# Performance work log

Hardware: AMD Instinct MI355X
Metric: run time of the kernel (lower is better)

## Reference

```python
import jax, jax.numpy as jnp
import numpy as np

B, T, F, H = 2048, 512, 60, 7  # batch, seq_len, input_size, hidden_size


def setup_inputs() -> dict:
    key = jax.random.key(0)
    ks = jax.random.split(key, 9)
    bound = 1.0 / np.sqrt(H)  # PyTorch LSTM init: U(-1/sqrt(H), 1/sqrt(H))
    u = lambda k, s: jax.random.uniform(k, s, jnp.float32, -bound, bound)
    return {
        "x": jax.random.normal(ks[0], (B, T, F), jnp.float32),
        "Wih0": u(ks[1], (4 * H, F)),
        "Whh0": u(ks[2], (4 * H, H)),
        "bih0": u(ks[3], (4 * H,)),
        "bhh0": u(ks[4], (4 * H,)),
        "Wih1": u(ks[5], (4 * H, H)),
        "Whh1": u(ks[6], (4 * H, H)),
        "bih1": u(ks[7], (4 * H,)),
        "bhh1": u(ks[8], (4 * H,)),
    }


def _cell(xt, h, c, Wih, Whh, b):
    # PyTorch gate order: input, forget, cell(g), output
    gates = xt @ Wih.T + h @ Whh.T + b  # [B, 4H]
    i, f, g, o = jnp.split(gates, 4, axis=-1)
    c_new = jax.nn.sigmoid(f) * c + jax.nn.sigmoid(i) * jnp.tanh(g)
    h_new = jax.nn.sigmoid(o) * jnp.tanh(c_new)
    return h_new, c_new


def reference(x, Wih0, Whh0, bih0, bhh0, Wih1, Whh1, bih1, bhh1):
    b0 = bih0 + bhh0
    b1 = bih1 + bhh1
    batch = x.shape[0]
    hid = Whh0.shape[1]
    z = jnp.zeros((batch, hid), x.dtype)

    def step(carry, xt):
        h0, c0, h1, c1 = carry
        h0, c0 = _cell(xt, h0, c0, Wih0, Whh0, b0)
        h1, c1 = _cell(h0, h1, c1, Wih1, Whh1, b1)
        return (h0, c0, h1, c1), None

    xs = jnp.swapaxes(x, 0, 1)  # [T, B, F] for scan over time
    (h0, c0, h1, c1), _ = jax.lax.scan(step, (z, z, z, z), xs)
    # out[:, -1] of batch_first LSTM == final hidden state of top layer
    return h1
```

## Files before the change

kernel.cpp:

```cpp
#include <hip/hip_runtime.h>


#define B_ 2048
#define T_ 512
#define F_ 60
#define H_ 7
#define G4 28
#define BT_ (B_ * T_)
#define L2E 1.4426950408889634f
#define PD 8

#if __has_builtin(__builtin_amdgcn_exp2f)
#define EXP2(x) __builtin_amdgcn_exp2f(x)
#else
#define EXP2(x) exp2f(x)
#endif

__device__ __forceinline__ float rcpf_(float v) { return __builtin_amdgcn_rcpf(v); }

__device__ __forceinline__ float bcast(float v, int srclane) {
    return __uint_as_float(__builtin_amdgcn_readlane(__float_as_uint(v), srclane));
}

__device__ __forceinline__ float dot7(const float* w, const float* h, float seed) {
    float m01 = fmaf(w[1], h[1], w[0] * h[0]);
    float m23 = fmaf(w[3], h[3], w[2] * h[2]);
    float m45 = fmaf(w[5], h[5], w[4] * h[4]);
    float m6  = fmaf(w[6], h[6], seed);
    return (m01 + m23) + (m45 + m6);
}

__global__ __launch_bounds__(256)
void proj_kernel(const float* __restrict__ x, const float* __restrict__ Wih0,
                 const float* __restrict__ bih0, const float* __restrict__ bhh0,
                 float* __restrict__ A)
{
    __shared__ float wsm[G4 * F_];
    __shared__ float bsm[G4];

    for (int i = threadIdx.x; i < G4 * F_; i += 256) wsm[i] = Wih0[i];
    if (threadIdx.x < G4) bsm[threadIdx.x] = bih0[threadIdx.x] + bhh0[threadIdx.x];
    __syncthreads();

    const int bt = blockIdx.x * 256 + threadIdx.x;

    float xr[F_];
    const float4* __restrict__ xp = (const float4*)(x + (size_t)bt * F_);
    #pragma unroll
    for (int j = 0; j < 15; ++j) {
        float4 q = xp[j];
        xr[4 * j + 0] = q.x; xr[4 * j + 1] = q.y;
        xr[4 * j + 2] = q.z; xr[4 * j + 3] = q.w;
    }

    float4* __restrict__ Ap = (float4*)(A + (size_t)bt * G4);
    #pragma unroll
    for (int rg = 0; rg < 7; ++rg) {
        float s[4];
        #pragma unroll
        for (int q = 0; q < 4; ++q) {
            const int r = rg * 4 + q;
            const float* w = &wsm[r * F_];
            float a0 = bsm[r], a1 = 0.f, a2 = 0.f, a3 = 0.f;
            #pragma unroll
            for (int k = 0; k < F_; k += 4) {
                a0 = fmaf(w[k + 0], xr[k + 0], a0);
                a1 = fmaf(w[k + 1], xr[k + 1], a1);
                a2 = fmaf(w[k + 2], xr[k + 2], a2);
                a3 = fmaf(w[k + 3], xr[k + 3], a3);
            }
            s[q] = (a0 + a1) + (a2 + a3);
        }
        Ap[rg] = make_float4(s[0], s[1], s[2], s[3]);
    }
}

__global__ __launch_bounds__(256)
void rec_kernel(const float* __restrict__ A,
                const float* __restrict__ Whh0,
                const float* __restrict__ Wih1, const float* __restrict__ Whh1,
                const float* __restrict__ bih1, const float* __restrict__ bhh1,
                float* __restrict__ out)
{
    const int tid   = threadIdx.x;
    const int lane  = tid & 63;
    const bool isL1 = lane >= 32;
    const int g     = lane & 31;
    const int r     = (g < G4) ? g : (G4 - 1);
    const int b     = blockIdx.x * 4 + (tid >> 6);

    float wA[H_], wB[H_];
    #pragma unroll
    for (int v = 0; v < H_; ++v) {
        wA[v] = isL1 ? Wih1[r * H_ + v] : Whh0[r * H_ + v];
        wB[v] = isL1 ? Whh1[r * H_ + v] : 0.f;
    }
    const float bias1 = bih1[r] + bhh1[r];

    const bool isT = (r >= 2 * H_ && r < 3 * H_);
    const float KK = isT ? (-2.f * L2E) : (-L2E);
    const float Aa = isT ? 2.f : 1.f;
    const float Ca = isT ? -1.f : 0.f;

    float h0v[H_] = {0, 0, 0, 0, 0, 0, 0};
    float h1v[H_] = {0, 0, 0, 0, 0, 0, 0};
    float c = 0.f, hnew = 0.f;

    const float* __restrict__ pa = A + (size_t)b * T_ * G4 + r;

    float buf[PD];
    #pragma unroll
    for (int i = 0; i < PD; ++i) buf[i] = pa[i * G4];

    for (int tt = 0; tt < T_; tt += PD) {
        #pragma unroll
        for (int s = 0; s < PD; ++s) {
            const int t = tt + s;
            const int tn = (t + PD < T_) ? (t + PD) : (T_ - 1);
            float nb = pa[(size_t)tn * G4];

            float seed = isL1 ? bias1 : buf[s];
            float a = dot7(wA, h0v, seed);
            a = dot7(wB, h1v, a);
            float act = fmaf(Aa, rcpf_(1.f + EXP2(KK * a)), Ca);

            float fg = __shfl(act, lane + 7, 64);
            float gg = __shfl(act, lane + 14, 64);
            float og = __shfl(act, lane + 21, 64);

            float cnew = fmaf(fg, c, act * gg);
            if (t == 0) cnew = isL1 ? 0.f : cnew;
            c = cnew;
            float th = fmaf(2.f, rcpf_(1.f + EXP2(-2.f * L2E * c)), -1.f);
            hnew = og * th;

            #pragma unroll
            for (int v = 0; v < H_; ++v) h0v[v] = bcast(hnew, v);
            #pragma unroll
            for (int v = 0; v < H_; ++v) h1v[v] = bcast(hnew, 32 + v);

            buf[s] = nb;
        }
    }

    {
        float a = dot7(wA, h0v, isL1 ? bias1 : 0.f);
        a = dot7(wB, h1v, a);
        float act = fmaf(Aa, rcpf_(1.f + EXP2(KK * a)), Ca);
        float fg = __shfl(act, lane + 7, 64);
        float gg = __shfl(act, lane + 14, 64);
        float og = __shfl(act, lane + 21, 64);
        c = fmaf(fg, c, act * gg);
        float th = fmaf(2.f, rcpf_(1.f + EXP2(-2.f * L2E * c)), -1.f);
        hnew = og * th;
    }

    if (isL1 && g < H_) out[(size_t)b * H_ + g] = hnew;
}

#define CH 16
#define NCH (T_ / CH)
#define F4 15
#define ROW4 (CH * F4)
#define BPB 4
#define TOT4 (BPB * ROW4)

__device__ __forceinline__ float proj32(const float* pw, const float4* rp, float seed) {
    float s0 = seed, s1 = 0.f, s2 = 0.f, s3 = 0.f;
    #pragma unroll
    for (int j = 0; j < 8; ++j) {
        float4 q = rp[j];
        s0 = fmaf(pw[4 * j + 0], q.x, s0);
        s1 = fmaf(pw[4 * j + 1], q.y, s1);
        s2 = fmaf(pw[4 * j + 2], q.z, s2);
        s3 = fmaf(pw[4 * j + 3], q.w, s3);
    }
    return (s0 + s1) + (s2 + s3);
}

__global__ __launch_bounds__(256, 2)
void lstm2_fallback(const float* __restrict__ x,
                    const float* __restrict__ Wih0, const float* __restrict__ Whh0,
                    const float* __restrict__ bih0, const float* __restrict__ bhh0,
                    const float* __restrict__ Wih1, const float* __restrict__ Whh1,
                    const float* __restrict__ bih1, const float* __restrict__ bhh1,
                    float* __restrict__ out)
{
    __shared__ float4 lds4[2][BPB][ROW4];

    const int tid   = threadIdx.x;
    const int lane  = tid & 63;
    const bool isL1 = lane >= 32;
    const int g     = lane & 31;
    const int r     = (g < G4) ? g : (G4 - 1);
    const int grp   = tid >> 6;
    const int b     = blockIdx.x * BPB + grp;

    float pw[32];
    {
        const int offs = isL1 ? 28 : 0;
        #pragma unroll
        for (int k = 0; k < 32; ++k) pw[k] = Wih0[r * F_ + offs + k];
        if (isL1) { pw[0] = pw[1] = pw[2] = pw[3] = 0.f; }
    }
    float wA[H_], wB[H_];
    #pragma unroll
    for (int v = 0; v < H_; ++v) {
        wA[v] = isL1 ? Wih1[r * H_ + v] : Whh0[r * H_ + v];
        wB[v] = isL1 ? Whh1[r * H_ + v] : 0.f;
    }
    const float bias0 = bih0[r] + bhh0[r];
    const float bias1 = bih1[r] + bhh1[r];

    const bool isT = (r >= 2 * H_ && r < 3 * H_);
    const float KK = isT ? (-2.f * L2E) : (-L2E);
    const float Aa = isT ? 2.f : 1.f;
    const float Ca = isT ? -1.f : 0.f;

    float h0v[H_] = {0, 0, 0, 0, 0, 0, 0};
    float h1v[H_] = {0, 0, 0, 0, 0, 0, 0};
    float c = 0.f, hnew = 0.f;

    const float4* __restrict__ xb =
        (const float4*)(x + (size_t)(blockIdx.x * BPB) * T_ * F_);
    const int XB4 = T_ * F4;
    const int lofs = isL1 ? 7 : 0;
    const float pseed = isL1 ? 0.f : bias0;

    #pragma unroll
    for (int i = 0; i < 4; ++i) {
        int idx = tid + 256 * i;
        if (idx < TOT4) {
            int bl = idx / ROW4;
            int j  = idx - bl * ROW4;
            lds4[0][bl][j] = xb[bl * XB4 + j];
        }
    }
    __syncthreads();

    float a_in;
    {
        float ow = proj32(pw, &lds4[0][grp][0] + lofs, pseed);
        a_in = ow + __shfl(ow, lane ^ 32, 64);
    }

    for (int ch = 0; ch < NCH; ++ch) {
        const int cn = (ch < NCH - 1) ? ch + 1 : ch;
        float4 st[4];
        #pragma unroll
        for (int i = 0; i < 4; ++i) {
            int idx = tid + 256 * i;
            if (idx < TOT4) {
                int bl = idx / ROW4;
                int j  = idx - bl * ROW4;
                st[i] = xb[bl * XB4 + cn * ROW4 + j];
            }
        }

        const int buf = ch & 1;
        const float4* __restrict__ rowb = &lds4[buf][grp][0] + lofs;

        #pragma unroll
        for (int s = 0; s < CH; ++s) {
            float seed = isL1 ? bias1 : a_in;
            float a = dot7(wA, h0v, seed);
            a = dot7(wB, h1v, a);
            float act = fmaf(Aa, rcpf_(1.f + EXP2(KK * a)), Ca);

            float fg = __shfl(act, lane + 7, 64);
            float gg = __shfl(act, lane + 14, 64);
            float og = __shfl(act, lane + 21, 64);

            float cnew = fmaf(fg, c, act * gg);
            if (ch == 0 && s == 0) cnew = isL1 ? 0.f : cnew;
            c = cnew;
            float th = fmaf(2.f, rcpf_(1.f + EXP2(-2.f * L2E * c)), -1.f);
            hnew = og * th;

            #pragma unroll
            for (int v = 0; v < H_; ++v) h0v[v] = bcast(hnew, v);
            if (ch > 0 || s > 0) {
                #pragma unroll
                for (int v = 0; v < H_; ++v) h1v[v] = bcast(hnew, 32 + v);
            }

            if (s < CH - 1) {
                float ow = proj32(pw, rowb + (s + 1) * F4, pseed);
                a_in = ow + __shfl(ow, lane ^ 32, 64);
            }
        }

        #pragma unroll
        for (int i = 0; i < 4; ++i) {
            int idx = tid + 256 * i;
            if (idx < TOT4) {
                int bl = idx / ROW4;
                int j  = idx - bl * ROW4;
                lds4[buf ^ 1][bl][j] = st[i];
            }
        }
        __syncthreads();

        if (ch < NCH - 1) {
            float ow = proj32(pw, &lds4[buf ^ 1][grp][0] + lofs, pseed);
            a_in = ow + __shfl(ow, lane ^ 32, 64);
        }
    }

    {
        float a = dot7(wA, h0v, isL1 ? bias1 : 0.f);
        a = dot7(wB, h1v, a);
        float act = fmaf(Aa, rcpf_(1.f + EXP2(KK * a)), Ca);
        float fg = __shfl(act, lane + 7, 64);
        float gg = __shfl(act, lane + 14, 64);
        float og = __shfl(act, lane + 21, 64);
        c = fmaf(fg, c, act * gg);
        float th = fmaf(2.f, rcpf_(1.f + EXP2(-2.f * L2E * c)), -1.f);
        hnew = og * th;
    }

    if (isL1 && g < H_) out[(size_t)b * H_ + g] = hnew;
}

extern "C" void kernel_launch(void* const* d_in, const int* in_sizes, int n_in,
                              void* d_out, int out_size, void* d_ws, size_t ws_size,
                              hipStream_t stream) {
    const float* x    = (const float*)d_in[0];
    const float* Wih0 = (const float*)d_in[1];
    const float* Whh0 = (const float*)d_in[2];
    const float* bih0 = (const float*)d_in[3];
    const float* bhh0 = (const float*)d_in[4];
    const float* Wih1 = (const float*)d_in[5];
    const float* Whh1 = (const float*)d_in[6];
    const float* bih1 = (const float*)d_in[7];
    const float* bhh1 = (const float*)d_in[8];
    float* out = (float*)d_out;

    const size_t need = (size_t)BT_ * G4 * sizeof(float);
    if (ws_size >= need) {
        float* A = (float*)d_ws;
        proj_kernel<<<dim3(BT_ / 256), dim3(256), 0, stream>>>(x, Wih0, bih0, bhh0, A);
        rec_kernel<<<dim3(B_ / 4), dim3(256), 0, stream>>>(A, Whh0, Wih1, Whh1,
                                                           bih1, bhh1, out);
    } else {
        lstm2_fallback<<<dim3(B_ / BPB), dim3(256), 0, stream>>>(
            x, Wih0, Whh0, bih0, bhh0, Wih1, Whh1, bih1, bhh1, out);
    }
}
```

Baseline: 541.0 us.

## Fuse input projection into recurrent kernel with producer/consumer warp specialization

Replaces the separate projection kernel and its global workspace with one fused kernel. Four producer waves compute the input projection for 64-step chunks into double-buffered LDS while four recurrence waves consume the previous chunk. This removes the global write and read-back of the projected gates (about 117 MB). The cost is a block-wide barrier every chunk, and the serial recurrence now depends on the producer keeping pace. Each producer lane computes a 28x60 dot product per timestep, and grid occupancy is limited to 512 blocks.

Measured after the change: 923.5 us. 1.71x slower.

```diff
diff --git a/kernel.cpp b/kernel.cpp
--- a/kernel.cpp
+++ b/kernel.cpp
@@ -6,9 +6,10 @@
 #define F_ 60
 #define H_ 7
 #define G4 28
-#define BT_ (B_ * T_)
 #define L2E 1.4426950408889634f
-#define PD 8
+#define PD 4
+#define CHK 64
+#define NCHK (T_ / CHK)
 
 #if __has_builtin(__builtin_amdgcn_exp2f)
 #define EXP2(x) __builtin_amdgcn_exp2f(x)
@@ -30,120 +31,135 @@
     return (m01 + m23) + (m45 + m6);
 }
 
-__global__ __launch_bounds__(256)
-void proj_kernel(const float* __restrict__ x, const float* __restrict__ Wih0,
-                 const float* __restrict__ bih0, const float* __restrict__ bhh0,
-                 float* __restrict__ A)
+__device__ __forceinline__ void produce(const float* __restrict__ x,
+                                        const float* __restrict__ wsm,
+                                        const float* __restrict__ bsm,
+                                        float (*__restrict__ dst)[G4],
+                                        int bb, int ck, int lane)
 {
-    __shared__ float wsm[G4 * F_];
-    __shared__ float bsm[G4];
-
-    for (int i = threadIdx.x; i < G4 * F_; i += 256) wsm[i] = Wih0[i];
-    if (threadIdx.x < G4) bsm[threadIdx.x] = bih0[threadIdx.x] + bhh0[threadIdx.x];
-    __syncthreads();
-
-    const int bt = blockIdx.x * 256 + threadIdx.x;
-
+    const float4* __restrict__ xp =
+        (const float4*)(x + ((size_t)bb * T_ + ck * CHK + lane) * F_);
     float xr[F_];
-    const float4* __restrict__ xp = (const float4*)(x + (size_t)bt * F_);
     #pragma unroll
     for (int j = 0; j < 15; ++j) {
         float4 q = xp[j];
         xr[4 * j + 0] = q.x; xr[4 * j + 1] = q.y;
         xr[4 * j + 2] = q.z; xr[4 * j + 3] = q.w;
     }
-
-    float4* __restrict__ Ap = (float4*)(A + (size_t)bt * G4);
     #pragma unroll
-    for (int rg = 0; rg < 7; ++rg) {
-        float s[4];
+    for (int r = 0; r < G4; ++r) {
+        const float* w = &wsm[r * F_];
+        float a0 = bsm[r], a1 = 0.f, a2 = 0.f, a3 = 0.f;
         #pragma unroll
-        for (int q = 0; q < 4; ++q) {
-            const int r = rg * 4 + q;
-            const float* w = &wsm[r * F_];
-            float a0 = bsm[r], a1 = 0.f, a2 = 0.f, a3 = 0.f;
-            #pragma unroll
-            for (int k = 0; k < F_; k += 4) {
-                a0 = fmaf(w[k + 0], xr[k + 0], a0);
-                a1 = fmaf(w[k + 1], xr[k + 1], a1);
-                a2 = fmaf(w[k + 2], xr[k + 2], a2);
-                a3 = fmaf(w[k + 3], xr[k + 3], a3);
-            }
-            s[q] = (a0 + a1) + (a2 + a3);
+        for (int k = 0; k < F_; k += 4) {
+            a0 = fmaf(w[k + 0], xr[k + 0], a0);
+            a1 = fmaf(w[k + 1], xr[k + 1], a1);
+            a2 = fmaf(w[k + 2], xr[k + 2], a2);
+            a3 = fmaf(w[k + 3], xr[k + 3], a3);
         }
-        Ap[rg] = make_float4(s[0], s[1], s[2], s[3]);
+        dst[lane][r] = (a0 + a1) + (a2 + a3);
     }
 }
 
-__global__ __launch_bounds__(256)
-void rec_kernel(const float* __restrict__ A,
-                const float* __restrict__ Whh0,
+__global__ __launch_bounds__(512, 4)
+void lstm_fused(const float* __restrict__ x,
+                const float* __restrict__ Wih0, const float* __restrict__ Whh0,
+                const float* __restrict__ bih0, const float* __restrict__ bhh0,
                 const float* __restrict__ Wih1, const float* __restrict__ Whh1,
                 const float* __restrict__ bih1, const float* __restrict__ bhh1,
                 float* __restrict__ out)
 {
+    __shared__ float Abuf[2][4][CHK][G4];
+    __shared__ float wsm[G4 * F_];
+    __shared__ float bsm[G4];
+
     const int tid   = threadIdx.x;
     const int lane  = tid & 63;
+    const int wv    = tid >> 6;
+    const bool isRec = (wv < 4);
+    const int  bw   = wv & 3;
+    const int  b    = blockIdx.x * 4 + bw;
+
+    if (!isRec) {
+        const int tp = tid - 256;
+        for (int i = tp; i < G4 * F_; i += 256) wsm[i] = Wih0[i];
+        if (tp < G4) bsm[tp] = bih0[tp] + bhh0[tp];
+    }
+
     const bool isL1 = lane >= 32;
-    const int g     = lane & 31;
-    const int r     = (g < G4) ? g : (G4 - 1);
-    const int b     = blockIdx.x * 4 + (tid >> 6);
+    const int  g    = lane & 31;
+    const int  r    = (g < G4) ? g : (G4 - 1);
 
     float wA[H_], wB[H_];
-    #pragma unroll
-    for (int v = 0; v < H_; ++v) {
-        wA[v] = isL1 ? Wih1[r * H_ + v] : Whh0[r * H_ + v];
-        wB[v] = isL1 ? Whh1[r * H_ + v] : 0.f;
-    }
-    const float bias1 = bih1[r] + bhh1[r];
-
+    float bias1 = 0.f;
+    float h0v[H_] = {0, 0, 0, 0, 0, 0, 0};
+    float h1v[H_] = {0, 0, 0, 0, 0, 0, 0};
+    float c = 0.f, hnew = 0.f;
     const bool isT = (r >= 2 * H_ && r < 3 * H_);
     const float KK = isT ? (-2.f * L2E) : (-L2E);
     const float Aa = isT ? 2.f : 1.f;
     const float Ca = isT ? -1.f : 0.f;
 
-    float h0v[H_] = {0, 0, 0, 0, 0, 0, 0};
-    float h1v[H_] = {0, 0, 0, 0, 0, 0, 0};
-    float c = 0.f, hnew = 0.f;
-
-    const float* __restrict__ pa = A + (size_t)b * T_ * G4 + r;
-
-    float buf[PD];
-    #pragma unroll
-    for (int i = 0; i < PD; ++i) buf[i] = pa[i * G4];
-
-    for (int tt = 0; tt < T_; tt += PD) {
+    if (isRec) {
         #pragma unroll
-        for (int s = 0; s < PD; ++s) {
-            const int t = tt + s;
-            const int tn = (t + PD < T_) ? (t + PD) : (T_ - 1);
-            float nb = pa[(size_t)tn * G4];
-
-            float seed = isL1 ? bias1 : buf[s];
-            float a = dot7(wA, h0v, seed);
-            a = dot7(wB, h1v, a);
-            float act = fmaf(Aa, rcpf_(1.f + EXP2(KK * a)), Ca);
-
-            float fg = __shfl(act, lane + 7, 64);
-            float gg = __shfl(act, lane + 14, 64);
-            float og = __shfl(act, lane + 21, 64);
-
-            float cnew = fmaf(fg, c, act * gg);
-            if (t == 0) cnew = isL1 ? 0.f : cnew;
-            c = cnew;
-            float th = fmaf(2.f, rcpf_(1.f + EXP2(-2.f * L2E * c)), -1.f);
-            hnew = og * th;
-
-            #pragma unroll
-            for (int v = 0; v < H_; ++v) h0v[v] = bcast(hnew, v);
-            #pragma unroll
-            for (int v = 0; v < H_; ++v) h1v[v] = bcast(hnew, 32 + v);
-
-            buf[s] = nb;
+        for (int v = 0; v < H_; ++v) {
+            wA[v] = isL1 ? Wih1[r * H_ + v] : Whh0[r * H_ + v];
+            wB[v] = isL1 ? Whh1[r * H_ + v] : 0.f;
         }
+        bias1 = bih1[r] + bhh1[r];
     }
 
-    {
+    __syncthreads();
+
+    if (!isRec) produce(x, wsm, bsm, Abuf[0][bw], b, 0, lane);
+    __syncthreads();
+
+    for (int ck = 0; ck < NCHK; ++ck) {
+        const int pb = ck & 1;
+        if (isRec) {
+            const float* __restrict__ Ab = &Abuf[pb][bw][0][r];
+            float sbuf[PD];
+            #pragma unroll
+            for (int i = 0; i < PD; ++i) sbuf[i] = Ab[i * G4];
+
+            for (int tt = 0; tt < CHK; tt += PD) {
+                #pragma unroll
+                for (int s = 0; s < PD; ++s) {
+                    const int tl = tt + s;
+                    const int tn = (tl + PD < CHK) ? (tl + PD) : (CHK - 1);
+                    float nb = Ab[tn * G4];
+                    const int t = ck * CHK + tl;
+
+                    float seed = isL1 ? bias1 : sbuf[s];
+                    float a = dot7(wA, h0v, seed);
+                    a = dot7(wB, h1v, a);
+                    float act = fmaf(Aa, rcpf_(1.f + EXP2(KK * a)), Ca);
+
+                    float fg = __shfl(act, lane + 7, 64);
+                    float gg = __shfl(act, lane + 14, 64);
+                    float og = __shfl(act, lane + 21, 64);
+
+                    float cnew = fmaf(fg, c, act * gg);
+                    if (t == 0) cnew = isL1 ? 0.f : cnew;
+                    c = cnew;
+                    float th = fmaf(2.f, rcpf_(1.f + EXP2(-2.f * L2E * c)), -1.f);
+                    hnew = og * th;
+
+                    #pragma unroll
+                    for (int v = 0; v < H_; ++v) h0v[v] = bcast(hnew, v);
+                    #pragma unroll
+                    for (int v = 0; v < H_; ++v) h1v[v] = bcast(hnew, 32 + v);
+
+                    sbuf[s] = nb;
+                }
+            }
+        } else if (ck + 1 < NCHK) {
+            produce(x, wsm, bsm, Abuf[pb ^ 1][bw], b, ck + 1, lane);
+        }
+        __syncthreads();
+    }
+
+    if (isRec) {
         float a = dot7(wA, h0v, isL1 ? bias1 : 0.f);
         a = dot7(wB, h1v, a);
         float act = fmaf(Aa, rcpf_(1.f + EXP2(KK * a)), Ca);
@@ -153,173 +169,9 @@
         c = fmaf(fg, c, act * gg);
         float th = fmaf(2.f, rcpf_(1.f + EXP2(-2.f * L2E * c)), -1.f);
         hnew = og * th;
+
+        if (isL1 && g < H_) out[(size_t)b * H_ + g] = hnew;
     }
-
-    if (isL1 && g < H_) out[(size_t)b * H_ + g] = hnew;
-}
-
-#define CH 16
-#define NCH (T_ / CH)
-#define F4 15
-#define ROW4 (CH * F4)
-#define BPB 4
-#define TOT4 (BPB * ROW4)
-
-__device__ __forceinline__ float proj32(const float* pw, const float4* rp, float seed) {
-    float s0 = seed, s1 = 0.f, s2 = 0.f, s3 = 0.f;
-    #pragma unroll
-    for (int j = 0; j < 8; ++j) {
-        float4 q = rp[j];
-        s0 = fmaf(pw[4 * j + 0], q.x, s0);
-        s1 = fmaf(pw[4 * j + 1], q.y, s1);
-        s2 = fmaf(pw[4 * j + 2], q.z, s2);
-        s3 = fmaf(pw[4 * j + 3], q.w, s3);
-    }
-    return (s0 + s1) + (s2 + s3);
-}
-
-__global__ __launch_bounds__(256, 2)
-void lstm2_fallback(const float* __restrict__ x,
-                    const float* __restrict__ Wih0, const float* __restrict__ Whh0,
-                    const float* __restrict__ bih0, const float* __restrict__ bhh0,
-                    const float* __restrict__ Wih1, const float* __restrict__ Whh1,
-                    const float* __restrict__ bih1, const float* __restrict__ bhh1,
-                    float* __restrict__ out)
-{
-    __shared__ float4 lds4[2][BPB][ROW4];
-
-    const int tid   = threadIdx.x;
-    const int lane  = tid & 63;
-    const bool isL1 = lane >= 32;
-    const int g     = lane & 31;
-    const int r     = (g < G4) ? g : (G4 - 1);
-    const int grp   = tid >> 6;
-    const int b     = blockIdx.x * BPB + grp;
-
-    float pw[32];
-    {
-        const int offs = isL1 ? 28 : 0;
-        #pragma unroll
-        for (int k = 0; k < 32; ++k) pw[k] = Wih0[r * F_ + offs + k];
-        if (isL1) { pw[0] = pw[1] = pw[2] = pw[3] = 0.f; }
-    }
-    float wA[H_], wB[H_];
-    #pragma unroll
-    for (int v = 0; v < H_; ++v) {
-        wA[v] = isL1 ? Wih1[r * H_ + v] : Whh0[r * H_ + v];
-        wB[v] = isL1 ? Whh1[r * H_ + v] : 0.f;
-    }
-    const float bias0 = bih0[r] + bhh0[r];
-    const float bias1 = bih1[r] + bhh1[r];
-
-    const bool isT = (r >= 2 * H_ && r < 3 * H_);
-    const float KK = isT ? (-2.f * L2E) : (-L2E);
-    const float Aa = isT ? 2.f : 1.f;
-    const float Ca = isT ? -1.f : 0.f;
-
-    float h0v[H_] = {0, 0, 0, 0, 0, 0, 0};
-    float h1v[H_] = {0, 0, 0, 0, 0, 0, 0};
-    float c = 0.f, hnew = 0.f;
-
-    const float4* __restrict__ xb =
-        (const float4*)(x + (size_t)(blockIdx.x * BPB) * T_ * F_);
-    const int XB4 = T_ * F4;
-    const int lofs = isL1 ? 7 : 0;
-    const float pseed = isL1 ? 0.f : bias0;
-
-    #pragma unroll
-    for (int i = 0; i < 4; ++i) {
-        int idx = tid + 256 * i;
-        if (idx < TOT4) {
-            int bl = idx / ROW4;
-            int j  = idx - bl * ROW4;
-            lds4[0][bl][j] = xb[bl * XB4 + j];
-        }
-    }
-    __syncthreads();
-
-    float a_in;
-    {
-        float ow = proj32(pw, &lds4[0][grp][0] + lofs, pseed);
-        a_in = ow + __shfl(ow, lane ^ 32, 64);
-    }
-
-    for (int ch = 0; ch < NCH; ++ch) {
-        const int cn = (ch < NCH - 1) ? ch + 1 : ch;
-        float4 st[4];
-        #pragma unroll
-        for (int i = 0; i < 4; ++i) {
-            int idx = tid + 256 * i;
-            if (idx < TOT4) {
-                int bl = idx / ROW4;
-                int j  = idx - bl * ROW4;
-                st[i] = xb[bl * XB4 + cn * ROW4 + j];
-            }
-        }
-
-        const int buf = ch & 1;
-        const float4* __restrict__ rowb = &lds4[buf][grp][0] + lofs;
-
-        #pragma unroll
-        for (int s = 0; s < CH; ++s) {
-            float seed = isL1 ? bias1 : a_in;
-            float a = dot7(wA, h0v, seed);
-            a = dot7(wB, h1v, a);
-            float act = fmaf(Aa, rcpf_(1.f + EXP2(KK * a)), Ca);
-
-            float fg = __shfl(act, lane + 7, 64);
-            float gg = __shfl(act, lane + 14, 64);
-            float og = __shfl(act, lane + 21, 64);
-
-            float cnew = fmaf(fg, c, act * gg);
-            if (ch == 0 && s == 0) cnew = isL1 ? 0.f : cnew;
-            c = cnew;
-            float th = fmaf(2.f, rcpf_(1.f + EXP2(-2.f * L2E * c)), -1.f);
-            hnew = og * th;
-
-            #pragma unroll
-            for (int v = 0; v < H_; ++v) h0v[v] = bcast(hnew, v);
-            if (ch > 0 || s > 0) {
-                #pragma unroll
-                for (int v = 0; v < H_; ++v) h1v[v] = bcast(hnew, 32 + v);
-            }
-
-            if (s < CH - 1) {
-                float ow = proj32(pw, rowb + (s + 1) * F4, pseed);
-                a_in = ow + __shfl(ow, lane ^ 32, 64);
-            }
-        }
-
-        #pragma unroll
-        for (int i = 0; i < 4; ++i) {
-            int idx = tid + 256 * i;
-            if (idx < TOT4) {
-                int bl = idx / ROW4;
-                int j  = idx - bl * ROW4;
-                lds4[buf ^ 1][bl][j] = st[i];
-            }
-        }
-        __syncthreads();
-
-        if (ch < NCH - 1) {
-            float ow = proj32(pw, &lds4[buf ^ 1][grp][0] + lofs, pseed);
-            a_in = ow + __shfl(ow, lane ^ 32, 64);
-        }
-    }
-
-    {
-        float a = dot7(wA, h0v, isL1 ? bias1 : 0.f);
-        a = dot7(wB, h1v, a);
-        float act = fmaf(Aa, rcpf_(1.f + EXP2(KK * a)), Ca);
-        float fg = __shfl(act, lane + 7, 64);
-        float gg = __shfl(act, lane + 14, 64);
-        float og = __shfl(act, lane + 21, 64);
-        c = fmaf(fg, c, act * gg);
-        float th = fmaf(2.f, rcpf_(1.f + EXP2(-2.f * L2E * c)), -1.f);
-        hnew = og * th;
-    }
-
-    if (isL1 && g < H_) out[(size_t)b * H_ + g] = hnew;
 }
 
 extern "C" void kernel_launch(void* const* d_in, const int* in_sizes, int n_in,
@@ -336,14 +188,6 @@
     const float* bhh1 = (const float*)d_in[8];
     float* out = (float*)d_out;
 
-    const size_t need = (size_t)BT_ * G4 * sizeof(float);
-    if (ws_size >= need) {
-        float* A = (float*)d_ws;
-        proj_kernel<<<dim3(BT_ / 256), dim3(256), 0, stream>>>(x, Wih0, bih0, bhh0, A);
-        rec_kernel<<<dim3(B_ / 4), dim3(256), 0, stream>>>(A, Whh0, Wih1, Whh1,
-                                                           bih1, bhh1, out);
-    } else {
-        lstm2_fallback<<<dim3(B_ / BPB), dim3(256), 0, stream>>>(
-            x, Wih0, Whh0, bih0, bhh0, Wih1, Whh1, bih1, bhh1, out);
-    }
+    lstm_fused<<<dim3(B_ / 4), dim3(512), 0, stream>>>(
+        x, Wih0, Whh0, bih0, bhh0, Wih1, Whh1, bih1, bhh1, out);
 }
```
